# Kernel tuning notes

Measured on AMD Instinct MI355X. Metric: run time of the kernel, lower is better.

Reference implementation:

```python
import jax, jax.numpy as jnp
import numpy as np

L = 5  # number of attention+MLP stages

def _layernorm(x, g, b, eps=1e-5):
    mu = x.mean(-1, keepdims=True)
    var = ((x - mu) ** 2).mean(-1, keepdims=True)
    return (x - mu) * jax.lax.rsqrt(var + eps) * g + b

def setup_inputs() -> dict:
    key = jax.random.key(0)
    B, N, C = 8, 2048, 512  # win_size=4, num_slices=12 -> C = 4*4*384//12 = 512
    ks = jax.random.split(key, 7)
    s = 0.02
    return {
        "x": jax.random.normal(ks[0], (B, N, C), dtype=jnp.float32),
        "qkv_w": jax.random.normal(ks[1], (L, C, 3 * C), dtype=jnp.float32) * s,
        "qkv_b": jnp.zeros((L, 3 * C), dtype=jnp.float32),
        "ln_g": jnp.ones((L, C), dtype=jnp.float32),
        "ln_b": jnp.zeros((L, C), dtype=jnp.float32),
        "fc1_w": jax.random.normal(ks[2], (L, C, 2 * C), dtype=jnp.float32) * s,
        "fc1_b": jnp.zeros((L, 2 * C), dtype=jnp.float32),
        "fc2_w": jax.random.normal(ks[3], (L, 2 * C, C), dtype=jnp.float32) * s,
        "fc2_b": jnp.zeros((L, C), dtype=jnp.float32),
    }

def reference(x, qkv_w, qkv_b, ln_g, ln_b, fc1_w, fc1_b, fc2_w, fc2_b):
    B, N, C = x.shape
    half = N // 2
    scale = C ** -0.5  # num_heads = 1 -> head_dim = C
    # Custom block mask: top-left (half x half) block fully visible,
    # top-right block masked; bottom half is tril with diagonal = N//2,
    # i.e. global row i >= half may attend to columns j <= i.
    i = jnp.arange(N)[:, None]
    j = jnp.arange(N)[None, :]
    allowed = jnp.where(i < half, j < half, j <= i)
    bias = jnp.where(allowed, 0.0, -1000.0).astype(x.dtype)  # (N, N)
    for l in range(L):
        # Mask3dAttention (single head)
        qkv = x @ qkv_w[l] + qkv_b[l]                      # (B, N, 3C)
        q, k, v = jnp.split(qkv, 3, axis=-1)               # each (B, N, C)
        attn = jnp.einsum("bnc,bmc->bnm", q * scale, k) + bias
        attn = jax.nn.softmax(attn, axis=-1)
        x = jnp.einsum("bnm,bmc->bnc", attn, v)
        # residual MLP on normed features
        y = _layernorm(x, ln_g[l], ln_b[l])
        h = jax.nn.gelu(y @ fc1_w[l] + fc1_b[l], approximate=False)
        x = x + (h @ fc2_w[l] + fc2_b[l])
    return x
```

## Files before the change

kernel.cpp:

```cpp
#include <hip/hip_runtime.h>
#include <math.h>

typedef unsigned short u16;
typedef __attribute__((ext_vector_type(8))) short bf16x8;
typedef __attribute__((ext_vector_type(4))) float f32x4;
typedef __attribute__((ext_vector_type(4))) unsigned short u16x4;

#define NLAYERS 5
#define BATCH 8
#define SEQ 2048
#define CH 512
#define ROWS_TOTAL (BATCH * SEQ)
#define HALF (SEQ / 2)
#define QSCALE_EXP2 0.06375871529f
#define EXP2_CAP 86.56f

#define SMEM_U16 32768
#define QK2_U16 24576

__device__ __forceinline__ u16 f2bf(float f) {
    unsigned u = __float_as_uint(f);
    u += 0x7fffu + ((u >> 16) & 1u);
    return (u16)(u >> 16);
}

__device__ __forceinline__ unsigned pk2(float a, float b) {
    unsigned r;
    asm("v_cvt_pk_bf16_f32 %0, %1, %2" : "=v"(r) : "v"(a), "v"(b));
    return r;
}

__device__ __forceinline__ u16x4 pack4(f32x4 v) {
    union { unsigned u[2]; u16x4 o; } r;
    r.u[0] = pk2(v[0], v[1]);
    r.u[1] = pk2(v[2], v[3]);
    return r.o;
}

__device__ __forceinline__ void st16(u16* p, u16x4 v) { *(u16x4*)p = v; }
__device__ __forceinline__ void st16f(float* p, f32x4 v) { *(f32x4*)p = v; }

__device__ __forceinline__ float fexp2(float x) {
    float r;
    asm("v_exp_f32 %0, %1" : "=v"(r) : "v"(x));
    return r;
}

__device__ __forceinline__ void llds16(const u16* g, u16* l) {
    __builtin_amdgcn_global_load_lds(
        (const __attribute__((address_space(1))) unsigned int*)g,
        (__attribute__((address_space(3))) unsigned int*)l, 16, 0, 0);
}

__device__ __forceinline__ void xcd_rc(int& rt, int& ct) {
    const int n = blockIdx.x;
    const int m = n >> 3;
    rt = (n & 7) * 16 + (m & 15);
    ct = m >> 4;
}

__device__ __forceinline__ void mm_issue(const u16* gA, const u16* gB,
                                         u16* lA, u16* lB, int lda, int ldb)
{
#pragma unroll
    for (int i = 0; i < 4; ++i)
        llds16(gA + (size_t)i * 32 * lda, lA + i * 2048);
#pragma unroll
    for (int i = 0; i < 4; ++i)
        llds16(gB + (size_t)i * 32 * ldb, lB + i * 2048);
}

__device__ __forceinline__ void mm_compute(const u16* As, const u16* Bs,
                                           const int aoff[2][4],
                                           const int boff[2][4],
                                           f32x4 acc[4][4])
{
#pragma unroll
    for (int h = 0; h < 2; ++h) {
        bf16x8 af[4], bfv[4];
#pragma unroll
        for (int t = 0; t < 4; ++t) af[t]  = *(const bf16x8*)&As[aoff[h][t]];
#pragma unroll
        for (int t = 0; t < 4; ++t) bfv[t] = *(const bf16x8*)&Bs[boff[h][t]];
#pragma unroll
        for (int ti = 0; ti < 4; ++ti)
#pragma unroll
            for (int tj = 0; tj < 4; ++tj)
                acc[ti][tj] = __builtin_amdgcn_mfma_f32_16x16x32_bf16(
                    af[ti], bfv[tj], acc[ti][tj], 0, 0, 0);
    }
}

__device__ __forceinline__ void mm_core(
    const u16* __restrict__ A, int lda,
    const u16* __restrict__ Bt, int ldb,
    int row0, int col0, int K,
    u16* SM, f32x4 acc[4][4])
{
    const int tid  = threadIdx.x;
    const int wave = tid >> 6, lane = tid & 63;
    const int wm = (wave & 1) * 64, wn = (wave >> 1) * 64;
    const int q  = lane >> 4,  ln = lane & 15;

    const int sr8 = lane >> 3;
    const int sc  = (lane & 7) ^ sr8;
    const u16* gA = A  + (size_t)(row0 + wave * 8 + sr8) * lda + sc * 8;
    const u16* gB = Bt + (size_t)(col0 + wave * 8 + sr8) * ldb + sc * 8;

    u16* const A0 = SM;
    u16* const B0 = SM + 8192;
    u16* const A1 = SM + 16384;
    u16* const B1 = SM + 24576;
    u16* const w0a = A0 + wave * 512;
    u16* const w0b = B0 + wave * 512;
    u16* const w1a = A1 + wave * 512;
    u16* const w1b = B1 + wave * 512;

    int aoff[2][4], boff[2][4];
#pragma unroll
    for (int h = 0; h < 2; ++h) {
        const int pos = (((h * 4 + q) ^ (ln & 7)) * 8);
#pragma unroll
        for (int t = 0; t < 4; ++t) {
            aoff[h][t] = (wm + t * 16 + ln) * 64 + pos;
            boff[h][t] = (wn + t * 16 + ln) * 64 + pos;
        }
    }

#pragma unroll
    for (int ti = 0; ti < 4; ++ti)
#pragma unroll
        for (int tj = 0; tj < 4; ++tj)
#pragma unroll
            for (int e = 0; e < 4; ++e) acc[ti][tj][e] = 0.f;

    mm_issue(gA, gB, w0a, w0b, lda, ldb);
    gA += 64; gB += 64;

    for (int k0 = 0; k0 < K; k0 += 128) {
        if (k0 + 64 < K) {
            mm_issue(gA, gB, w1a, w1b, lda, ldb);
            gA += 64; gB += 64;
            asm volatile("s_waitcnt vmcnt(8)" ::: "memory");
        } else {
            asm volatile("s_waitcnt vmcnt(0)" ::: "memory");
        }
        __builtin_amdgcn_s_barrier();
        mm_compute(A0, B0, aoff, boff, acc);
        __builtin_amdgcn_s_barrier();
        __builtin_amdgcn_sched_barrier(0);
        if (k0 + 128 < K) {
            mm_issue(gA, gB, w0a, w0b, lda, ldb);
            gA += 64; gB += 64;
            asm volatile("s_waitcnt vmcnt(8)" ::: "memory");
        } else {
            asm volatile("s_waitcnt vmcnt(0)" ::: "memory");
        }
        __builtin_amdgcn_s_barrier();
        mm_compute(A1, B1, aoff, boff, acc);
        __builtin_amdgcn_s_barrier();
        __builtin_amdgcn_sched_barrier(0);
    }
}

template <typename F>
__device__ __forceinline__ void epi_emit(f32x4 acc[4][4], float* eb, F emit)
{
    const int tid = threadIdx.x, wave = tid >> 6, lane = tid & 63;
    const int wn = (wave >> 1) * 64;
    const int q = lane >> 4, ln = lane & 15;
#pragma unroll
    for (int p = 0; p < 4; ++p) {
        __syncthreads();
        if ((wave & 1) == (p >> 1)) {
            const int tibase = (p & 1) * 2;
#pragma unroll
            for (int tj = 0; tj < 4; ++tj)
#pragma unroll
                for (int t2 = 0; t2 < 2; ++t2)
#pragma unroll
                    for (int r = 0; r < 4; ++r)
                        eb[(t2 * 16 + q * 4 + r) * 132 + wn + tj * 16 + ln] =
                            acc[tibase + t2][tj][r];
        }
        __syncthreads();
#pragma unroll
        for (int s = 0; s < 4; ++s) {
            const int row = s * 8 + (tid >> 5);
            const int col = (tid & 31) * 4;
            f32x4 v = *(const f32x4*)&eb[row * 132 + col];
            emit(p * 32 + row, col, v);
        }
    }
}

__global__ __launch_bounds__(256) void qkv_gemm(
    const u16* __restrict__ A, const u16* __restrict__ Bt,
    const float* __restrict__ bias,
    u16* __restrict__ Qb, u16* __restrict__ Kb, u16* __restrict__ Vt,
    float* __restrict__ rowsum)
{
    __shared__ __align__(16) u16 SMEM[SMEM_U16];
    f32x4 acc[4][4];
    int rt, ct; xcd_rc(rt, ct);
    const int row0 = rt * 128, col0 = ct * 128;
    if (ct == 0 && threadIdx.x < 128)
        rowsum[row0 + threadIdx.x] = 0.f;
    mm_core(A, CH, Bt, CH, row0, col0, CH, SMEM, acc);

    if (ct < 8) {
        u16* dst = (ct < 4) ? Qb : Kb;
        const int cbase = (ct < 4) ? col0 : col0 - CH;
        const float sc = (ct < 4) ? QSCALE_EXP2 : 1.0f;
        epi_emit(acc, (float*)SMEM, [&](int row, int col, f32x4 v) {
            const float4 bb = *(const float4*)&bias[col0 + col];
            v[0] = (v[0] + bb.x) * sc; v[1] = (v[1] + bb.y) * sc;
            v[2] = (v[2] + bb.z) * sc; v[3] = (v[3] + bb.w) * sc;
            st16(&dst[(size_t)(row0 + row) * CH + cbase + col], pack4(v));
        });
    } else {
        const int tid = threadIdx.x, wave = tid >> 6, lane = tid & 63;
        const int wm = (wave & 1) * 64, wn = (wave >> 1) * 64;
        const int q = lane >> 4, ln = lane & 15;
#pragma unroll
        for (int tj = 0; tj < 4; ++tj) {
            const int gcol = col0 + wn + tj * 16 + ln;
            const float bv = bias[gcol];
#pragma unroll
            for (int ti = 0; ti < 4; ++ti) {
                const int grow = row0 + wm + ti * 16 + q * 4;
                const int b = grow >> 11, j = grow & (SEQ - 1);
                f32x4 vv;
                vv[0] = acc[ti][tj][0] + bv; vv[1] = acc[ti][tj][1] + bv;
                vv[2] = acc[ti][tj][2] + bv; vv[3] = acc[ti][tj][3] + bv;
                st16(&Vt[(size_t)b * CH * SEQ +
                         (size_t)(gcol - 2 * CH) * SEQ + j], pack4(vv));
            }
        }
    }
}

__global__ __launch_bounds__(512, 4) void qk2_gemm(
    const u16* __restrict__ Qb, const u16* __restrict__ Kb,
    u16* __restrict__ Sb, float* __restrict__ rowsum)
{
    __shared__ __align__(16) u16 SMEM[QK2_U16];
    u16* const As = SMEM;
    u16* const Bs = SMEM + 8192;
    float* const eb = (float*)SMEM;

    const int id = blockIdx.x;
    const int b = id & 7;
    int u = id >> 3, it, pr;
    if (u < 32) { it = u >> 2; pr = u & 3; }
    else {
        int v = u - 32; it = 8; int len = 5;
        while (v >= len) { v -= len; ++it; len = 5 + ((it - 8) >> 1); }
        pr = v;
    }

    const int tid = threadIdx.x;
    const int w = tid >> 6, lane = tid & 63;
    const int wq = w & 3;
    const int wm = (wq & 1) * 64;
    const int wn = (w >> 2) * 128 + (wq >> 1) * 64;
    const int q = lane >> 4, ln = lane & 15;
    const int sr8 = lane >> 3, sc = (lane & 7) ^ sr8;

    const int row0 = it * 128, col0 = pr * 256;
    const u16* const Qg = Qb + (size_t)b * SEQ * CH;
    const u16* const Kg = Kb + (size_t)b * SEQ * CH;
    u16* const S = Sb + (size_t)b * SEQ * SEQ;

    const u16* gA = Qg + (size_t)(row0 + w * 16 + sr8) * CH + sc * 8;
    const u16* gB = Kg + (size_t)(col0 + w * 32 + sr8) * CH + sc * 8;
    u16* const lA = As + w * 1024;
    u16* const lB = Bs + w * 2048;

    int aoff[2][4], boff[2][4];
#pragma unroll
    for (int h = 0; h < 2; ++h) {
        const int pos = (((h * 4 + q) ^ (ln & 7)) * 8);
#pragma unroll
        for (int t = 0; t < 4; ++t) {
            aoff[h][t] = (wm + t * 16 + ln) * 64 + pos;
            boff[h][t] = (wn + t * 16 + ln) * 64 + pos;
        }
    }

    f32x4 acc[4][4];
#pragma unroll
    for (int ti = 0; ti < 4; ++ti)
#pragma unroll
        for (int tj = 0; tj < 4; ++tj)
#pragma unroll
            for (int e = 0; e < 4; ++e) acc[ti][tj][e] = 0.f;

    for (int s = 0; s < 8; ++s) {
        __syncthreads();
        llds16(gA,               lA);
        llds16(gA +  8 * CH,     lA + 512);
        llds16(gB,               lB);
        llds16(gB +  8 * CH,     lB + 512);
        llds16(gB + 16 * CH,     lB + 1024);
        llds16(gB + 24 * CH,     lB + 1536);
        gA += 64; gB += 64;
        __syncthreads();
        mm_compute(As, Bs, aoff, boff, acc);
    }

    const bool upper = (it < 8);
#pragma unroll
    for (int p = 0; p < 4; ++p) {
        __syncthreads();
        if ((wq & 1) == (p >> 1)) {
            const int tibase = (p & 1) * 2;
#pragma unroll
            for (int tj = 0; tj < 4; ++tj)
#pragma unroll
                for (int t2 = 0; t2 < 2; ++t2)
#pragma unroll
                    for (int r = 0; r < 4; ++r)
                        eb[(t2 * 16 + q * 4 + r) * 260 + wn + tj * 16 + ln] =
                            acc[tibase + t2][tj][r];
        }
        __syncthreads();
#pragma unroll
        for (int s2 = 0; s2 < 4; ++s2) {
            const int row = s2 * 8 + w;
            const int col = lane * 4;
            f32x4 v = *(const f32x4*)&eb[row * 260 + col];
            const int grow = row0 + p * 32 + row;
            const int gcol = col0 + col;
            f32x4 pv;
#pragma unroll
            for (int e = 0; e < 4; ++e) {
                const bool allowed = upper || (gcol + e <= grow);
                pv[e] = allowed ? fexp2(fminf(v[e], EXP2_CAP)) : 0.f;
            }
            st16(&S[(size_t)grow * SEQ + gcol], pack4(pv));
            float rs = pv[0] + pv[1] + pv[2] + pv[3];
            rs += __shfl_xor(rs, 1, 64);
            rs += __shfl_xor(rs, 2, 64);
            rs += __shfl_xor(rs, 4, 64);
            rs += __shfl_xor(rs, 8, 64);
            rs += __shfl_xor(rs, 16, 64);
            rs += __shfl_xor(rs, 32, 64);
            if (lane == 0)
                atomicAdd(&rowsum[b * SEQ + grow], rs);
        }
    }
}

__global__ __launch_bounds__(256) void pv_gemm(
    const u16* __restrict__ Sb, const u16* __restrict__ Vt,
    const float* __restrict__ rowsum, float* __restrict__ O)
{
    const int n = blockIdx.x;
    const int b = n & 7, m = n >> 3;
    const int it = 15 - (m >> 2), ct = m & 3;
    const int Kfull = ((it < 8) ? 8 : (it + 1)) * 128;
    __shared__ __align__(16) u16 SMEM[SMEM_U16];
    f32x4 acc[4][4];
    const u16* A  = Sb + (size_t)b * SEQ * SEQ;
    const u16* Bt = Vt + (size_t)b * CH * SEQ;
    const int row0 = it * 128, col0 = ct * 128;
    mm_core(A, SEQ, Bt, SEQ, row0, col0, Kfull, SMEM, acc);

    epi_emit(acc, (float*)SMEM, [&](int row, int col, f32x4 v) {
        const int grow = row0 + row;
        const float rden = 1.0f / rowsum[b * SEQ + grow];
        v[0] *= rden; v[1] *= rden; v[2] *= rden; v[3] *= rden;
        st16f(&O[(size_t)(b * SEQ + grow) * CH + col0 + col], v);
    });
}

__global__ __launch_bounds__(256) void fc1_gemm(
    const u16* __restrict__ A, const u16* __restrict__ Bt,
    const float* __restrict__ bias, u16* __restrict__ H)
{
    __shared__ __align__(16) u16 SMEM[SMEM_U16];
    f32x4 acc[4][4];
    int rt, ct; xcd_rc(rt, ct);
    const int row0 = rt * 128, col0 = ct * 128;
    mm_core(A, CH, Bt, CH, row0, col0, CH, SMEM, acc);
    epi_emit(acc, (float*)SMEM, [&](int row, int col, f32x4 v) {
        const float4 bb = *(const float4*)&bias[col0 + col];
        v[0] += bb.x; v[1] += bb.y; v[2] += bb.z; v[3] += bb.w;
#pragma unroll
        for (int e = 0; e < 4; ++e)
            v[e] = 0.5f * v[e] * (1.f + erff(v[e] * 0.70710678118654752f));
        st16(&H[(size_t)(row0 + row) * (2 * CH) + col0 + col], pack4(v));
    });
}

template <bool WRITE_X>
__global__ __launch_bounds__(256) void fc2_gemm(
    const u16* __restrict__ A, const u16* __restrict__ Bt,
    const float* __restrict__ bias, float* __restrict__ X,
    u16* __restrict__ Xb)
{
    __shared__ __align__(16) u16 SMEM[SMEM_U16];
    f32x4 acc[4][4];
    int rt, ct; xcd_rc(rt, ct);
    const int row0 = rt * 128, col0 = ct * 128;
    mm_core(A, 2 * CH, Bt, 2 * CH, row0, col0, 2 * CH, SMEM, acc);
    epi_emit(acc, (float*)SMEM, [&](int row, int col, f32x4 v) {
        const size_t idx = (size_t)(row0 + row) * CH + col0 + col;
        const float4 bb = *(const float4*)&bias[col0 + col];
        const f32x4 xv = *(const f32x4*)&X[idx];
        v[0] += bb.x + xv[0]; v[1] += bb.y + xv[1];
        v[2] += bb.z + xv[2]; v[3] += bb.w + xv[3];
        if (WRITE_X) st16f(&X[idx], v);
        st16(&Xb[idx], pack4(v));
    });
}

__device__ __forceinline__ float block_sum(float v, volatile float* red, int tid)
{
#pragma unroll
    for (int off = 1; off < 64; off <<= 1) v += __shfl_xor(v, off, 64);
    __syncthreads();
    if ((tid & 63) == 0) red[tid >> 6] = v;
    __syncthreads();
    return red[0] + red[1] + red[2] + red[3];
}

__global__ __launch_bounds__(256) void ln_kernel(
    const float* __restrict__ x, const float* __restrict__ g,
    const float* __restrict__ bta, u16* __restrict__ y)
{
    __shared__ float red[4];
    const int tid = threadIdx.x;
    const size_t base = (size_t)blockIdx.x * CH;
    float x0 = x[base + tid];
    float x1 = x[base + 256 + tid];
    float mu = block_sum(x0 + x1, red, tid) * (1.f / CH);
    float d0 = x0 - mu, d1 = x1 - mu;
    float var = block_sum(d0 * d0 + d1 * d1, red, tid) * (1.f / CH);
    float w = 1.f / sqrtf(var + 1e-5f);
    const float y0 = d0 * w * g[tid]       + bta[tid];
    const float y1 = d1 * w * g[256 + tid] + bta[256 + tid];
    const unsigned pk = pk2(y0, y1);
    y[base + tid]       = (u16)(pk & 0xffffu);
    y[base + 256 + tid] = (u16)(pk >> 16);
}

__global__ __launch_bounds__(256) void f2bf_kernel(
    const float* __restrict__ in, u16* __restrict__ out)
{
    const int i = blockIdx.x * 256 + threadIdx.x;
    float4 vv = ((const float4*)in)[i];
    f32x4 v; v[0] = vv.x; v[1] = vv.y; v[2] = vv.z; v[3] = vv.w;
    u16x4 o = pack4(v);
    *(u16x4*)&out[(size_t)i * 4] = o;
}

__global__ __launch_bounds__(256) void wtrans_kernel(
    const float* __restrict__ in, u16* __restrict__ out, int K, int N)
{
    __shared__ float tile[32][33];
    const int l = blockIdx.z;
    in  += (size_t)l * K * N;
    out += (size_t)l * K * N;
    const int n0 = blockIdx.x * 32, k0 = blockIdx.y * 32;
    const int r = threadIdx.x >> 3, c4 = (threadIdx.x & 7) * 4;
    float4 v = *(const float4*)&in[(size_t)(k0 + r) * N + n0 + c4];
    tile[r][c4 + 0] = v.x; tile[r][c4 + 1] = v.y;
    tile[r][c4 + 2] = v.z; tile[r][c4 + 3] = v.w;
    __syncthreads();
    f32x4 t;
    t[0] = tile[c4 + 0][r]; t[1] = tile[c4 + 1][r];
    t[2] = tile[c4 + 2][r]; t[3] = tile[c4 + 3][r];
    st16(&out[(size_t)(n0 + r) * K + k0 + c4], pack4(t));
}

extern "C" void kernel_launch(void* const* d_in, const int* in_sizes, int n_in,
                              void* d_out, int out_size, void* d_ws, size_t ws_size,
                              hipStream_t stream)
{
    const float* x_in  = (const float*)d_in[0];
    const float* qkv_w = (const float*)d_in[1];
    const float* qkv_b = (const float*)d_in[2];
    const float* ln_g  = (const float*)d_in[3];
    const float* ln_b  = (const float*)d_in[4];
    const float* fc1_w = (const float*)d_in[5];
    const float* fc1_b = (const float*)d_in[6];
    const float* fc2_w = (const float*)d_in[7];
    const float* fc2_b = (const float*)d_in[8];

    float* xbuf = (float*)d_out;

    char* p = (char*)d_ws;
    u16* qkv_wt = (u16*)p; p += (size_t)NLAYERS * 1536 * 512 * 2;
    u16* fc1_wt = (u16*)p; p += (size_t)NLAYERS * 1024 * 512 * 2;
    u16* fc2_wt = (u16*)p; p += (size_t)NLAYERS * 512 * 1024 * 2;
    u16* xb = (u16*)p; p += (size_t)ROWS_TOTAL * CH * 2;
    u16* Qb = (u16*)p; p += (size_t)ROWS_TOTAL * CH * 2;
    u16* Kb = (u16*)p; p += (size_t)ROWS_TOTAL * CH * 2;
    u16* Vt = (u16*)p; p += (size_t)ROWS_TOTAL * CH * 2;
    float* rowsum = (float*)p; p += (size_t)ROWS_TOTAL * 4;
    u16* Sb = (u16*)p;
    u16* yb = Sb;
    u16* hb = Sb + (size_t)ROWS_TOTAL * CH;

    const dim3 blk(256);
    const dim3 blk2(512);

    f2bf_kernel<<<dim3(ROWS_TOTAL * CH / 1024), blk, 0, stream>>>(x_in, xb);
    wtrans_kernel<<<dim3(1536 / 32, 512 / 32, NLAYERS), blk, 0, stream>>>(
        qkv_w, qkv_wt, 512, 1536);
    wtrans_kernel<<<dim3(1024 / 32, 512 / 32, NLAYERS), blk, 0, stream>>>(
        fc1_w, fc1_wt, 512, 1024);
    wtrans_kernel<<<dim3(512 / 32, 1024 / 32, NLAYERS), blk, 0, stream>>>(
        fc2_w, fc2_wt, 1024, 512);

    for (int l = 0; l < NLAYERS; ++l) {
        qkv_gemm<<<dim3(128 * 12), blk, 0, stream>>>(
            xb, qkv_wt + (size_t)l * 1536 * 512, qkv_b + (size_t)l * 1536,
            Qb, Kb, Vt, rowsum);
        qk2_gemm<<<dim3(672), blk2, 0, stream>>>(Qb, Kb, Sb, rowsum);
        pv_gemm<<<dim3(512), blk, 0, stream>>>(Sb, Vt, rowsum, xbuf);
        ln_kernel<<<dim3(ROWS_TOTAL), blk, 0, stream>>>(
            xbuf, ln_g + (size_t)l * CH, ln_b + (size_t)l * CH, yb);
        fc1_gemm<<<dim3(128 * 8), blk, 0, stream>>>(
            yb, fc1_wt + (size_t)l * 1024 * 512, fc1_b + (size_t)l * 1024, hb);
        if (l < NLAYERS - 1)
            fc2_gemm<false><<<dim3(128 * 4), blk, 0, stream>>>(
                hb, fc2_wt + (size_t)l * 512 * 1024, fc2_b + (size_t)l * 512,
                xbuf, xb);
        else
            fc2_gemm<true><<<dim3(128 * 4), blk, 0, stream>>>(
                hb, fc2_wt + (size_t)l * 512 * 1024, fc2_b + (size_t)l * 512,
                xbuf, xb);
    }
}
```

Measured before the change: 980.5 us.

## Port QKV, FC1 and FC2 GEMMs to 512-thread 128x256 tile core

Pulls the 512-thread, 128x256-tile main loop and epilogue out of the QK score kernel into shared helpers (mm2_core, epi_emit2). The QKV, FC1 and FC2 projection GEMMs now use them instead of the 256-thread 128x128 kernels, halving their grid sizes. The aim is more reuse of each loaded A tile, and better latency hiding from 8 waves per block with K-step 64. The tradeoff is fewer blocks per launch (fc2 drops to 256, about one wave over the CUs) and a different shared-memory staging scheme.

```diff
diff --git a/kernel.cpp b/kernel.cpp
--- a/kernel.cpp
+++ b/kernel.cpp
@@ -16,7 +16,7 @@
 #define EXP2_CAP 86.56f
 
 #define SMEM_U16 32768
-#define QK2_U16 24576
+#define PAIR_U16 24576
 
 __device__ __forceinline__ u16 f2bf(float f) {
     unsigned u = __float_as_uint(f);
@@ -52,24 +52,6 @@
         (__attribute__((address_space(3))) unsigned int*)l, 16, 0, 0);
 }
 
-__device__ __forceinline__ void xcd_rc(int& rt, int& ct) {
-    const int n = blockIdx.x;
-    const int m = n >> 3;
-    rt = (n & 7) * 16 + (m & 15);
-    ct = m >> 4;
-}
-
-__device__ __forceinline__ void mm_issue(const u16* gA, const u16* gB,
-                                         u16* lA, u16* lB, int lda, int ldb)
-{
-#pragma unroll
-    for (int i = 0; i < 4; ++i)
-        llds16(gA + (size_t)i * 32 * lda, lA + i * 2048);
-#pragma unroll
-    for (int i = 0; i < 4; ++i)
-        llds16(gB + (size_t)i * 32 * ldb, lB + i * 2048);
-}
-
 __device__ __forceinline__ void mm_compute(const u16* As, const u16* Bs,
                                            const int aoff[2][4],
                                            const int boff[2][4],
@@ -89,6 +71,249 @@
                 acc[ti][tj] = __builtin_amdgcn_mfma_f32_16x16x32_bf16(
                     af[ti], bfv[tj], acc[ti][tj], 0, 0, 0);
     }
+}
+
+__device__ __forceinline__ void mm2_core(
+    const u16* __restrict__ A, int lda,
+    const u16* __restrict__ Bt, int ldb,
+    int row0, int col0, int K,
+    u16* SM, f32x4 acc[4][4])
+{
+    const int tid = threadIdx.x;
+    const int w = tid >> 6, lane = tid & 63;
+    const int wq = w & 3;
+    const int wm = (wq & 1) * 64;
+    const int wn = (w >> 2) * 128 + (wq >> 1) * 64;
+    const int q = lane >> 4, ln = lane & 15;
+    const int sr8 = lane >> 3, sc = (lane & 7) ^ sr8;
+
+    u16* const As = SM;
+    u16* const Bs = SM + 8192;
+    const u16* gA = A  + (size_t)(row0 + w * 16 + sr8) * lda + sc * 8;
+    const u16* gB = Bt + (size_t)(col0 + w * 32 + sr8) * ldb + sc * 8;
+    u16* const lA = As + w * 1024;
+    u16* const lB = Bs + w * 2048;
+
+    int aoff[2][4], boff[2][4];
+#pragma unroll
+    for (int h = 0; h < 2; ++h) {
+        const int pos = (((h * 4 + q) ^ (ln & 7)) * 8);
+#pragma unroll
+        for (int t = 0; t < 4; ++t) {
+            aoff[h][t] = (wm + t * 16 + ln) * 64 + pos;
+            boff[h][t] = (wn + t * 16 + ln) * 64 + pos;
+        }
+    }
+
+#pragma unroll
+    for (int ti = 0; ti < 4; ++ti)
+#pragma unroll
+        for (int tj = 0; tj < 4; ++tj)
+#pragma unroll
+            for (int e = 0; e < 4; ++e) acc[ti][tj][e] = 0.f;
+
+    for (int s = 0; s < (K >> 6); ++s) {
+        __syncthreads();
+        llds16(gA,                    lA);
+        llds16(gA + (size_t)8 * lda,  lA + 512);
+        llds16(gB,                    lB);
+        llds16(gB + (size_t)8 * ldb,  lB + 512);
+        llds16(gB + (size_t)16 * ldb, lB + 1024);
+        llds16(gB + (size_t)24 * ldb, lB + 1536);
+        gA += 64; gB += 64;
+        __syncthreads();
+        mm_compute(As, Bs, aoff, boff, acc);
+    }
+}
+
+template <typename F>
+__device__ __forceinline__ void epi_emit2(f32x4 acc[4][4], float* eb, F emit)
+{
+    const int tid = threadIdx.x, w = tid >> 6, lane = tid & 63;
+    const int wq = w & 3;
+    const int wn = (w >> 2) * 128 + (wq >> 1) * 64;
+    const int q = lane >> 4, ln = lane & 15;
+#pragma unroll
+    for (int p = 0; p < 4; ++p) {
+        __syncthreads();
+        if ((wq & 1) == (p >> 1)) {
+            const int tibase = (p & 1) * 2;
+#pragma unroll
+            for (int tj = 0; tj < 4; ++tj)
+#pragma unroll
+                for (int t2 = 0; t2 < 2; ++t2)
+#pragma unroll
+                    for (int r = 0; r < 4; ++r)
+                        eb[(t2 * 16 + q * 4 + r) * 260 + wn + tj * 16 + ln] =
+                            acc[tibase + t2][tj][r];
+        }
+        __syncthreads();
+#pragma unroll
+        for (int s2 = 0; s2 < 4; ++s2) {
+            const int row = s2 * 8 + w;
+            const int col = lane * 4;
+            f32x4 v = *(const f32x4*)&eb[row * 260 + col];
+            emit(p * 32 + row, col, v);
+        }
+    }
+}
+
+__global__ __launch_bounds__(512, 4) void qkv_gemm2(
+    const u16* __restrict__ A, const u16* __restrict__ Bt,
+    const float* __restrict__ bias,
+    u16* __restrict__ Qb, u16* __restrict__ Kb, u16* __restrict__ Vt,
+    float* __restrict__ rowsum)
+{
+    __shared__ __align__(16) u16 SMEM[PAIR_U16];
+    f32x4 acc[4][4];
+    const int id = blockIdx.x;
+    const int m = id >> 3;
+    const int rt = (id & 7) * 16 + (m & 15);
+    const int ctp = m >> 4;
+    const int row0 = rt * 128, col0 = ctp * 256;
+    if (ctp == 0 && threadIdx.x < 128)
+        rowsum[row0 + threadIdx.x] = 0.f;
+    mm2_core(A, CH, Bt, CH, row0, col0, CH, SMEM, acc);
+
+    if (ctp < 4) {
+        u16* dst = (ctp < 2) ? Qb : Kb;
+        const int cbase = (ctp < 2) ? col0 : col0 - CH;
+        const float sc = (ctp < 2) ? QSCALE_EXP2 : 1.0f;
+        epi_emit2(acc, (float*)SMEM, [&](int row, int col, f32x4 v) {
+            const float4 bb = *(const float4*)&bias[col0 + col];
+            v[0] = (v[0] + bb.x) * sc; v[1] = (v[1] + bb.y) * sc;
+            v[2] = (v[2] + bb.z) * sc; v[3] = (v[3] + bb.w) * sc;
+            st16(&dst[(size_t)(row0 + row) * CH + cbase + col], pack4(v));
+        });
+    } else {
+        const int tid = threadIdx.x, w = tid >> 6, lane = tid & 63;
+        const int wq = w & 3;
+        const int wm = (wq & 1) * 64;
+        const int wn = (w >> 2) * 128 + (wq >> 1) * 64;
+        const int q = lane >> 4, ln = lane & 15;
+#pragma unroll
+        for (int tj = 0; tj < 4; ++tj) {
+            const int gcol = col0 + wn + tj * 16 + ln;
+            const float bv = bias[gcol];
+#pragma unroll
+            for (int ti = 0; ti < 4; ++ti) {
+                const int grow = row0 + wm + ti * 16 + q * 4;
+                const int b = grow >> 11, j = grow & (SEQ - 1);
+                f32x4 vv;
+                vv[0] = acc[ti][tj][0] + bv; vv[1] = acc[ti][tj][1] + bv;
+                vv[2] = acc[ti][tj][2] + bv; vv[3] = acc[ti][tj][3] + bv;
+                st16(&Vt[(size_t)b * CH * SEQ +
+                         (size_t)(gcol - 2 * CH) * SEQ + j], pack4(vv));
+            }
+        }
+    }
+}
+
+__global__ __launch_bounds__(512, 4) void qk2_gemm(
+    const u16* __restrict__ Qb, const u16* __restrict__ Kb,
+    u16* __restrict__ Sb, float* __restrict__ rowsum)
+{
+    __shared__ __align__(16) u16 SMEM[PAIR_U16];
+    float* const eb = (float*)SMEM;
+
+    const int id = blockIdx.x;
+    const int b = id & 7;
+    int u = id >> 3, it, pr;
+    if (u < 32) { it = u >> 2; pr = u & 3; }
+    else {
+        int v = u - 32; it = 8; int len = 5;
+        while (v >= len) { v -= len; ++it; len = 5 + ((it - 8) >> 1); }
+        pr = v;
+    }
+
+    const int row0 = it * 128, col0 = pr * 256;
+    const u16* const Qg = Qb + (size_t)b * SEQ * CH;
+    const u16* const Kg = Kb + (size_t)b * SEQ * CH;
+    u16* const S = Sb + (size_t)b * SEQ * SEQ;
+
+    f32x4 acc[4][4];
+    mm2_core(Qg, CH, Kg, CH, row0, col0, CH, SMEM, acc);
+
+    const bool upper = (it < 8);
+    const int lane = threadIdx.x & 63;
+    epi_emit2(acc, eb, [&](int row, int col, f32x4 v) {
+        const int grow = row0 + row;
+        const int gcol = col0 + col;
+        f32x4 pv;
+#pragma unroll
+        for (int e = 0; e < 4; ++e) {
+            const bool allowed = upper || (gcol + e <= grow);
+            pv[e] = allowed ? fexp2(fminf(v[e], EXP2_CAP)) : 0.f;
+        }
+        st16(&S[(size_t)grow * SEQ + gcol], pack4(pv));
+        float rs = pv[0] + pv[1] + pv[2] + pv[3];
+        rs += __shfl_xor(rs, 1, 64);
+        rs += __shfl_xor(rs, 2, 64);
+        rs += __shfl_xor(rs, 4, 64);
+        rs += __shfl_xor(rs, 8, 64);
+        rs += __shfl_xor(rs, 16, 64);
+        rs += __shfl_xor(rs, 32, 64);
+        if (lane == 0)
+            atomicAdd(&rowsum[b * SEQ + grow], rs);
+    });
+}
+
+__global__ __launch_bounds__(512, 4) void fc1_gemm2(
+    const u16* __restrict__ A, const u16* __restrict__ Bt,
+    const float* __restrict__ bias, u16* __restrict__ H)
+{
+    __shared__ __align__(16) u16 SMEM[PAIR_U16];
+    f32x4 acc[4][4];
+    const int id = blockIdx.x;
+    const int m = id >> 3;
+    const int rt = (id & 7) * 16 + (m & 15);
+    const int ctp = m >> 4;
+    const int row0 = rt * 128, col0 = ctp * 256;
+    mm2_core(A, CH, Bt, CH, row0, col0, CH, SMEM, acc);
+    epi_emit2(acc, (float*)SMEM, [&](int row, int col, f32x4 v) {
+        const float4 bb = *(const float4*)&bias[col0 + col];
+        v[0] += bb.x; v[1] += bb.y; v[2] += bb.z; v[3] += bb.w;
+#pragma unroll
+        for (int e = 0; e < 4; ++e)
+            v[e] = 0.5f * v[e] * (1.f + erff(v[e] * 0.70710678118654752f));
+        st16(&H[(size_t)(row0 + row) * (2 * CH) + col0 + col], pack4(v));
+    });
+}
+
+template <bool WRITE_X>
+__global__ __launch_bounds__(512, 4) void fc2_gemm2(
+    const u16* __restrict__ A, const u16* __restrict__ Bt,
+    const float* __restrict__ bias, float* __restrict__ X,
+    u16* __restrict__ Xb)
+{
+    __shared__ __align__(16) u16 SMEM[PAIR_U16];
+    f32x4 acc[4][4];
+    const int id = blockIdx.x;
+    const int m = id >> 3;
+    const int rt = (id & 7) * 16 + (m & 15);
+    const int ctp = m >> 4;
+    const int row0 = rt * 128, col0 = ctp * 256;
+    mm2_core(A, 2 * CH, Bt, 2 * CH, row0, col0, 2 * CH, SMEM, acc);
+    epi_emit2(acc, (float*)SMEM, [&](int row, int col, f32x4 v) {
+        const size_t idx = (size_t)(row0 + row) * CH + col0 + col;
+        const float4 bb = *(const float4*)&bias[col0 + col];
+        const f32x4 xv = *(const f32x4*)&X[idx];
+        v[0] += bb.x + xv[0]; v[1] += bb.y + xv[1];
+        v[2] += bb.z + xv[2]; v[3] += bb.w + xv[3];
+        if (WRITE_X) st16f(&X[idx], v);
+        st16(&Xb[idx], pack4(v));
+    });
+}
+
+__device__ __forceinline__ void mm_issue(const u16* gA, const u16* gB,
+                                         u16* lA, u16* lB, int lda, int ldb)
+{
+#pragma unroll
+    for (int i = 0; i < 4; ++i)
+        llds16(gA + (size_t)i * 32 * lda, lA + i * 2048);
+#pragma unroll
+    for (int i = 0; i < 4; ++i)
+        llds16(gB + (size_t)i * 32 * ldb, lB + i * 2048);
 }
 
 __device__ __forceinline__ void mm_core(
@@ -194,164 +419,6 @@
     }
 }
 
-__global__ __launch_bounds__(256) void qkv_gemm(
-    const u16* __restrict__ A, const u16* __restrict__ Bt,
-    const float* __restrict__ bias,
-    u16* __restrict__ Qb, u16* __restrict__ Kb, u16* __restrict__ Vt,
-    float* __restrict__ rowsum)
-{
-    __shared__ __align__(16) u16 SMEM[SMEM_U16];
-    f32x4 acc[4][4];
-    int rt, ct; xcd_rc(rt, ct);
-    const int row0 = rt * 128, col0 = ct * 128;
-    if (ct == 0 && threadIdx.x < 128)
-        rowsum[row0 + threadIdx.x] = 0.f;
-    mm_core(A, CH, Bt, CH, row0, col0, CH, SMEM, acc);
-
-    if (ct < 8) {
-        u16* dst = (ct < 4) ? Qb : Kb;
-        const int cbase = (ct < 4) ? col0 : col0 - CH;
-        const float sc = (ct < 4) ? QSCALE_EXP2 : 1.0f;
-        epi_emit(acc, (float*)SMEM, [&](int row, int col, f32x4 v) {
-            const float4 bb = *(const float4*)&bias[col0 + col];
-            v[0] = (v[0] + bb.x) * sc; v[1] = (v[1] + bb.y) * sc;
-            v[2] = (v[2] + bb.z) * sc; v[3] = (v[3] + bb.w) * sc;
-            st16(&dst[(size_t)(row0 + row) * CH + cbase + col], pack4(v));
-        });
-    } else {
-        const int tid = threadIdx.x, wave = tid >> 6, lane = tid & 63;
-        const int wm = (wave & 1) * 64, wn = (wave >> 1) * 64;
-        const int q = lane >> 4, ln = lane & 15;
-#pragma unroll
-        for (int tj = 0; tj < 4; ++tj) {
-            const int gcol = col0 + wn + tj * 16 + ln;
-            const float bv = bias[gcol];
-#pragma unroll
-            for (int ti = 0; ti < 4; ++ti) {
-                const int grow = row0 + wm + ti * 16 + q * 4;
-                const int b = grow >> 11, j = grow & (SEQ - 1);
-                f32x4 vv;
-                vv[0] = acc[ti][tj][0] + bv; vv[1] = acc[ti][tj][1] + bv;
-                vv[2] = acc[ti][tj][2] + bv; vv[3] = acc[ti][tj][3] + bv;
-                st16(&Vt[(size_t)b * CH * SEQ +
-                         (size_t)(gcol - 2 * CH) * SEQ + j], pack4(vv));
-            }
-        }
-    }
-}
-
-__global__ __launch_bounds__(512, 4) void qk2_gemm(
-    const u16* __restrict__ Qb, const u16* __restrict__ Kb,
-    u16* __restrict__ Sb, float* __restrict__ rowsum)
-{
-    __shared__ __align__(16) u16 SMEM[QK2_U16];
-    u16* const As = SMEM;
-    u16* const Bs = SMEM + 8192;
-    float* const eb = (float*)SMEM;
-
-    const int id = blockIdx.x;
-    const int b = id & 7;
-    int u = id >> 3, it, pr;
-    if (u < 32) { it = u >> 2; pr = u & 3; }
-    else {
-        int v = u - 32; it = 8; int len = 5;
-        while (v >= len) { v -= len; ++it; len = 5 + ((it - 8) >> 1); }
-        pr = v;
-    }
-
-    const int tid = threadIdx.x;
-    const int w = tid >> 6, lane = tid & 63;
-    const int wq = w & 3;
-    const int wm = (wq & 1) * 64;
-    const int wn = (w >> 2) * 128 + (wq >> 1) * 64;
-    const int q = lane >> 4, ln = lane & 15;
-    const int sr8 = lane >> 3, sc = (lane & 7) ^ sr8;
-
-    const int row0 = it * 128, col0 = pr * 256;
-    const u16* const Qg = Qb + (size_t)b * SEQ * CH;
-    const u16* const Kg = Kb + (size_t)b * SEQ * CH;
-    u16* const S = Sb + (size_t)b * SEQ * SEQ;
-
-    const u16* gA = Qg + (size_t)(row0 + w * 16 + sr8) * CH + sc * 8;
-    const u16* gB = Kg + (size_t)(col0 + w * 32 + sr8) * CH + sc * 8;
-    u16* const lA = As + w * 1024;
-    u16* const lB = Bs + w * 2048;
-
-    int aoff[2][4], boff[2][4];
-#pragma unroll
-    for (int h = 0; h < 2; ++h) {
-        const int pos = (((h * 4 + q) ^ (ln & 7)) * 8);
-#pragma unroll
-        for (int t = 0; t < 4; ++t) {
-            aoff[h][t] = (wm + t * 16 + ln) * 64 + pos;
-            boff[h][t] = (wn + t * 16 + ln) * 64 + pos;
-        }
-    }
-
-    f32x4 acc[4][4];
-#pragma unroll
-    for (int ti = 0; ti < 4; ++ti)
-#pragma unroll
-        for (int tj = 0; tj < 4; ++tj)
-#pragma unroll
-            for (int e = 0; e < 4; ++e) acc[ti][tj][e] = 0.f;
-
-    for (int s = 0; s < 8; ++s) {
-        __syncthreads();
-        llds16(gA,               lA);
-        llds16(gA +  8 * CH,     lA + 512);
-        llds16(gB,               lB);
-        llds16(gB +  8 * CH,     lB + 512);
-        llds16(gB + 16 * CH,     lB + 1024);
-        llds16(gB + 24 * CH,     lB + 1536);
-        gA += 64; gB += 64;
-        __syncthreads();
-        mm_compute(As, Bs, aoff, boff, acc);
-    }
-
-    const bool upper = (it < 8);
-#pragma unroll
-    for (int p = 0; p < 4; ++p) {
-        __syncthreads();
-        if ((wq & 1) == (p >> 1)) {
-            const int tibase = (p & 1) * 2;
-#pragma unroll
-            for (int tj = 0; tj < 4; ++tj)
-#pragma unroll
-                for (int t2 = 0; t2 < 2; ++t2)
-#pragma unroll
-                    for (int r = 0; r < 4; ++r)
-                        eb[(t2 * 16 + q * 4 + r) * 260 + wn + tj * 16 + ln] =
-                            acc[tibase + t2][tj][r];
-        }
-        __syncthreads();
-#pragma unroll
-        for (int s2 = 0; s2 < 4; ++s2) {
-            const int row = s2 * 8 + w;
-            const int col = lane * 4;
-            f32x4 v = *(const f32x4*)&eb[row * 260 + col];
-            const int grow = row0 + p * 32 + row;
-            const int gcol = col0 + col;
-            f32x4 pv;
-#pragma unroll
-            for (int e = 0; e < 4; ++e) {
-                const bool allowed = upper || (gcol + e <= grow);
-                pv[e] = allowed ? fexp2(fminf(v[e], EXP2_CAP)) : 0.f;
-            }
-            st16(&S[(size_t)grow * SEQ + gcol], pack4(pv));
-            float rs = pv[0] + pv[1] + pv[2] + pv[3];
-            rs += __shfl_xor(rs, 1, 64);
-            rs += __shfl_xor(rs, 2, 64);
-            rs += __shfl_xor(rs, 4, 64);
-            rs += __shfl_xor(rs, 8, 64);
-            rs += __shfl_xor(rs, 16, 64);
-            rs += __shfl_xor(rs, 32, 64);
-            if (lane == 0)
-                atomicAdd(&rowsum[b * SEQ + grow], rs);
-        }
-    }
-}
-
 __global__ __launch_bounds__(256) void pv_gemm(
     const u16* __restrict__ Sb, const u16* __restrict__ Vt,
     const float* __restrict__ rowsum, float* __restrict__ O)
@@ -372,47 +439,6 @@
         const float rden = 1.0f / rowsum[b * SEQ + grow];
         v[0] *= rden; v[1] *= rden; v[2] *= rden; v[3] *= rden;
         st16f(&O[(size_t)(b * SEQ + grow) * CH + col0 + col], v);
-    });
-}
-
-__global__ __launch_bounds__(256) void fc1_gemm(
-    const u16* __restrict__ A, const u16* __restrict__ Bt,
-    const float* __restrict__ bias, u16* __restrict__ H)
-{
-    __shared__ __align__(16) u16 SMEM[SMEM_U16];
-    f32x4 acc[4][4];
-    int rt, ct; xcd_rc(rt, ct);
-    const int row0 = rt * 128, col0 = ct * 128;
-    mm_core(A, CH, Bt, CH, row0, col0, CH, SMEM, acc);
-    epi_emit(acc, (float*)SMEM, [&](int row, int col, f32x4 v) {
-        const float4 bb = *(const float4*)&bias[col0 + col];
-        v[0] += bb.x; v[1] += bb.y; v[2] += bb.z; v[3] += bb.w;
-#pragma unroll
-        for (int e = 0; e < 4; ++e)
-            v[e] = 0.5f * v[e] * (1.f + erff(v[e] * 0.70710678118654752f));
-        st16(&H[(size_t)(row0 + row) * (2 * CH) + col0 + col], pack4(v));
-    });
-}
-
-template <bool WRITE_X>
-__global__ __launch_bounds__(256) void fc2_gemm(
-    const u16* __restrict__ A, const u16* __restrict__ Bt,
-    const float* __restrict__ bias, float* __restrict__ X,
-    u16* __restrict__ Xb)
-{
-    __shared__ __align__(16) u16 SMEM[SMEM_U16];
-    f32x4 acc[4][4];
-    int rt, ct; xcd_rc(rt, ct);
-    const int row0 = rt * 128, col0 = ct * 128;
-    mm_core(A, 2 * CH, Bt, 2 * CH, row0, col0, 2 * CH, SMEM, acc);
-    epi_emit(acc, (float*)SMEM, [&](int row, int col, f32x4 v) {
-        const size_t idx = (size_t)(row0 + row) * CH + col0 + col;
-        const float4 bb = *(const float4*)&bias[col0 + col];
-        const f32x4 xv = *(const f32x4*)&X[idx];
-        v[0] += bb.x + xv[0]; v[1] += bb.y + xv[1];
-        v[2] += bb.z + xv[2]; v[3] += bb.w + xv[3];
-        if (WRITE_X) st16f(&X[idx], v);
-        st16(&Xb[idx], pack4(v));
     });
 }
 
@@ -516,21 +542,21 @@
         fc2_w, fc2_wt, 1024, 512);
 
     for (int l = 0; l < NLAYERS; ++l) {
-        qkv_gemm<<<dim3(128 * 12), blk, 0, stream>>>(
+        qkv_gemm2<<<dim3(768), blk2, 0, stream>>>(
             xb, qkv_wt + (size_t)l * 1536 * 512, qkv_b + (size_t)l * 1536,
             Qb, Kb, Vt, rowsum);
         qk2_gemm<<<dim3(672), blk2, 0, stream>>>(Qb, Kb, Sb, rowsum);
         pv_gemm<<<dim3(512), blk, 0, stream>>>(Sb, Vt, rowsum, xbuf);
         ln_kernel<<<dim3(ROWS_TOTAL), blk, 0, stream>>>(
             xbuf, ln_g + (size_t)l * CH, ln_b + (size_t)l * CH, yb);
-        fc1_gemm<<<dim3(128 * 8), blk, 0, stream>>>(
+        fc1_gemm2<<<dim3(512), blk2, 0, stream>>>(
             yb, fc1_wt + (size_t)l * 1024 * 512, fc1_b + (size_t)l * 1024, hb);
         if (l < NLAYERS - 1)
-            fc2_gemm<false><<<dim3(128 * 4), blk, 0, stream>>>(
+            fc2_gemm2<false><<<dim3(256), blk2, 0, stream>>>(
                 hb, fc2_wt + (size_t)l * 512 * 1024, fc2_b + (size_t)l * 512,
                 xbuf, xb);
         else
-            fc2_gemm<true><<<dim3(128 * 4), blk, 0, stream>>>(
+            fc2_gemm2<true><<<dim3(256), blk2, 0, stream>>>(
                 hb, fc2_wt + (size_t)l * 512 * 1024, fc2_b + (size_t)l * 512,
                 xbuf, xb);
     }
```

New measurement: 995.2 us. No clear change (+1.5%).
